# Kernel tuning notes

Hardware: AMD Instinct MI355X
Metric: run time of the kernel (lower is better)

The kernel has to match this reference:

```python
import jax, jax.numpy as jnp
import numpy as np

B, H, N, D = 64, 12, 196, 768  # ViT-B/16 @ 224: 196 patch tokens + 1 CLS


def setup_inputs() -> dict:
    key = jax.random.key(0)
    k1, k2, k3 = jax.random.split(key, 3)
    student_tokens = jax.random.normal(k1, (B, N, D), dtype=jnp.float32)
    teacher_tokens = jax.random.normal(k2, (B, N, D), dtype=jnp.float32)
    teacher_attn = jax.random.uniform(k3, (B, H, N + 1, N + 1), dtype=jnp.float32)
    return {
        "student_tokens": student_tokens,
        "teacher_tokens": teacher_tokens,
        "teacher_attn": teacher_attn,
    }


def reference(student_tokens, teacher_tokens, teacher_attn):
    s = student_tokens.astype(jnp.float32)
    t = teacher_tokens.astype(jnp.float32)
    # CLS->patch attention, averaged over heads: [B, N]
    w = teacher_attn[:, :, 0, 1:].mean(axis=1)
    w = w / (w.sum(axis=-1, keepdims=True) + 1e-8)
    s = w[..., None] * s
    t = w[..., None] * t
    # center over token dim
    s_c = s - s.mean(axis=1, keepdims=True)
    t_c = t - t.mean(axis=1, keepdims=True)
    tr_s = jnp.sum(s_c * s_c, axis=(1, 2))  # [B]
    tr_t = jnp.sum(t_c * t_c, axis=(1, 2))  # [B]
    # cross-covariance: [B, D, D]
    cross = jnp.einsum("bnd,bne->bde", s_c, t_c)
    # nuclear norm = sum of singular values
    nuclear = jnp.linalg.svd(cross, compute_uv=False).sum(axis=-1)  # [B]
    loss = jnp.maximum(tr_s + tr_t - 2.0 * nuclear, 0.0).mean()
    return loss
```

## Files before the change

### kernel.cpp

```cpp
#include <hip/hip_runtime.h>
#include <hip/hip_bf16.h>
#include <math.h>

#define NTOK 196
#define NDIM 768
#define NB 64
#define NH 12
#define NA 197
#define MAT (NTOK * NTOK)
#define ATTN_HW (NA * NA)
#define POLAR_ITERS 15

#define PADC 208
#define NTILE 13
#define POLAR_LDS_BYTES (2 * NTOK * PADC * 2)

#define GCH 64
#define GPLANE (208 * GCH)
#define GRAM_LDS_BYTES (2 * GPLANE * 2)

#define FCH 64
#define FA_ROWS 208
#define FB_ROWS 112
#define FAPLANE (FA_ROWS * FCH)
#define FBPLANE (FB_ROWS * FCH)
#define FMF_LDS_BYTES ((2 * FAPLANE + 2 * FBPLANE) * 2)

#define POW_LD 197
#define POW_F_WORDS (NTOK * POW_LD)
#define POW_LDS_BYTES ((POW_F_WORDS + 2 * NTOK + 256) * 4)

#define PTLD 208
#define TRI_WORDS 19306
#define CHOL2_PT_WORDS (16 * PTLD)
#define CHOL2_TRI_OFF CHOL2_PT_WORDS
#define CHOL2_ROWOFF_OFF (CHOL2_TRI_OFF + TRI_WORDS)
#define CHOL2_PV_OFF 22832
#define CHOL2_LDS_BYTES ((CHOL2_PV_OFF + 32) * 4)

typedef __attribute__((ext_vector_type(8))) short short8;
typedef __attribute__((ext_vector_type(4))) short short4_t;
typedef __attribute__((ext_vector_type(4))) float f32x4;

__device__ inline short8 s8zero() { short8 z = {0,0,0,0,0,0,0,0}; return z; }

__device__ inline short f2bf(float f) {
  union { float f; unsigned u; } v; v.f = f;
  unsigned u = v.u;
  u += 0x7fffu + ((u >> 16) & 1u);
  return (short)(u >> 16);
}
__device__ inline float bf2f(short s) {
  union { unsigned u; float f; } v;
  v.u = ((unsigned)(unsigned short)s) << 16;
  return v.f;
}

__global__ void k_w(const float* __restrict__ attn, float* __restrict__ wbuf) {
  int b = blockIdx.x;
  int tid = threadIdx.x;
  __shared__ float red[256];
  float w0 = 0.f;
  if (tid < NTOK) {
    size_t base = (size_t)b * NH * ATTN_HW + 1 + tid;
    #pragma unroll
    for (int h = 0; h < NH; ++h) w0 += attn[base + (size_t)h * ATTN_HW];
    w0 *= (1.f / NH);
  }
  red[tid] = (tid < NTOK) ? w0 : 0.f;
  __syncthreads();
  for (int s = 128; s > 0; s >>= 1) { if (tid < s) red[tid] += red[tid + s]; __syncthreads(); }
  float S = red[0];
  if (tid < NTOK) wbuf[b * NTOK + tid] = w0 / (S + 1e-8f);
}

__global__ __launch_bounds__(512, 1) void k_gram_mfma(
    const float* __restrict__ s, const float* __restrict__ t,
    const float* __restrict__ wbuf, float* __restrict__ Gbuf) {
  extern __shared__ short gsm[];
  short* bhp = gsm;
  short* blp = gsm + GPLANE;
  __shared__ float wsh[NTOK];
  int slot = blockIdx.x, b = slot >> 1, src = slot & 1;
  const float* X = (src ? t : s) + (size_t)b * NTOK * NDIM;
  int tid = threadIdx.x;
  int wave = tid >> 6, ln15 = tid & 15, quad = (tid >> 4) & 3;

  if (tid < NTOK) wsh[tid] = wbuf[b * NTOK + tid];
  for (int i = tid; i < 768; i += 512) {
    int p = i / 384, o = i - p * 384;
    ((int*)(gsm + p * GPLANE + 196 * GCH))[o] = 0;
  }
  __syncthreads();

  f32x4 zz = {0.f, 0.f, 0.f, 0.f};
  f32x4 acc[12];
  #pragma unroll
  for (int j = 0; j < 12; ++j) acc[j] = zz;

  for (int c = 0; c < NDIM / GCH; ++c) {
    int kc = c * GCH;
    for (int gi = tid; gi < NTOK * 8; gi += 512) {
      int r = gi >> 3, g = gi & 7;
      const float* sp = X + (size_t)r * NDIM + kc + g * 8;
      float4 f0 = *(const float4*)(sp);
      float4 f1 = *(const float4*)(sp + 4);
      float wv = wsh[r];
      float vs[8] = {f0.x, f0.y, f0.z, f0.w, f1.x, f1.y, f1.z, f1.w};
      short8 hv, lv;
      #pragma unroll
      for (int e = 0; e < 8; ++e) {
        float y = wv * vs[e];
        short hb = f2bf(y);
        hv[e] = hb;
        lv[e] = f2bf(y - bf2f(hb));
      }
      int pg = (g ^ (r & 7)) * 8;
      *(short8*)(bhp + r * GCH + pg) = hv;
      *(short8*)(blp + r * GCH + pg) = lv;
    }
    __syncthreads();
    #pragma unroll
    for (int j = 0; j < 12; ++j) {
      int T = wave + 8 * j;
      if (T < 91) {
        int ti = (int)((sqrtf(8.f * T + 1.f) - 1.f) * 0.5f);
        if ((ti + 1) * (ti + 2) / 2 <= T) ++ti;
        if (ti * (ti + 1) / 2 > T) --ti;
        int tj = T - ti * (ti + 1) / 2;
        int ra = ti * 16 + ln15, rb = tj * 16 + ln15;
        #pragma unroll
        for (int ks = 0; ks < 2; ++ks) {
          int gb0 = ks * 4 + quad;
          int ga = (gb0 ^ (ra & 7)) * 8, gb = (gb0 ^ (rb & 7)) * 8;
          short8 ah = *(const short8*)(bhp + ra * GCH + ga);
          short8 al = *(const short8*)(blp + ra * GCH + ga);
          short8 bhf = *(const short8*)(bhp + rb * GCH + gb);
          short8 blf = *(const short8*)(blp + rb * GCH + gb);
          acc[j] = __builtin_amdgcn_mfma_f32_16x16x32_bf16(ah, bhf, acc[j], 0, 0, 0);
          acc[j] = __builtin_amdgcn_mfma_f32_16x16x32_bf16(ah, blf, acc[j], 0, 0, 0);
          acc[j] = __builtin_amdgcn_mfma_f32_16x16x32_bf16(al, bhf, acc[j], 0, 0, 0);
        }
      }
    }
    __syncthreads();
  }

  float* G = Gbuf + (size_t)slot * MAT;
  #pragma unroll
  for (int j = 0; j < 12; ++j) {
    int T = wave + 8 * j;
    if (T < 91) {
      int ti = (int)((sqrtf(8.f * T + 1.f) - 1.f) * 0.5f);
      if ((ti + 1) * (ti + 2) / 2 <= T) ++ti;
      if (ti * (ti + 1) / 2 > T) --ti;
      int tj = T - ti * (ti + 1) / 2;
      int col = tj * 16 + ln15;
      #pragma unroll
      for (int r = 0; r < 4; ++r) {
        int row = ti * 16 + quad * 4 + r;
        if (row < NTOK && col < NTOK) {
          G[row * NTOK + col] = acc[j][r];
          if (ti != tj) G[col * NTOK + row] = acc[j][r];
        }
      }
    }
  }
}

__global__ void k_center(float* __restrict__ Gbuf, float* __restrict__ trPb) {
  int slot = blockIdx.x;
  float* A = Gbuf + (size_t)slot * MAT;
  __shared__ float r[NTOK];
  __shared__ float red[256];
  __shared__ float gsh, dsh;
  int tid = threadIdx.x;
  float acc = 0.f;
  if (tid < NTOK) {
    for (int m = 0; m < NTOK; ++m) acc += A[m * NTOK + tid];
    r[tid] = acc * (1.f / NTOK);
  }
  red[tid] = (tid < NTOK) ? acc * (1.f / NTOK) : 0.f;
  __syncthreads();
  for (int s = 128; s > 0; s >>= 1) { if (tid < s) red[tid] += red[tid + s]; __syncthreads(); }
  float g = red[0] * (1.f / NTOK);
  float tv = (tid < NTOK) ? (A[tid * NTOK + tid] - 2.f * r[tid] + g) : 0.f;
  __syncthreads();
  red[tid] = tv;
  __syncthreads();
  for (int s = 128; s > 0; s >>= 1) { if (tid < s) red[tid] += red[tid + s]; __syncthreads(); }
  if (tid == 0) {
    float tr = red[0];
    trPb[slot] = tr;
    gsh = g;
    dsh = 1e-4f * fmaxf(tr, 0.f) * (1.f / NTOK);
  }
  __syncthreads();
  float gg = gsh, dd = dsh;
  for (int idx = tid; idx < MAT; idx += 256) {
    int n = idx / NTOK, m = idx - n * NTOK;
    float v = A[idx] - r[n] - r[m] + gg;
    if (n == m) v += dd;
    A[idx] = v;
  }
}

__global__ __launch_bounds__(256, 1) void k_chol_panel(float* __restrict__ Gbuf,
                                                       int transposeOut) {
  extern __shared__ float smf[];
  float* Pt = smf;
  float* tri = smf + CHOL2_TRI_OFF;
  int* rowoff = (int*)(smf + CHOL2_ROWOFF_OFF);
  float* pvb = smf + CHOL2_PV_OFF;
  int slot = blockIdx.x;
  float* A = Gbuf + (size_t)slot * MAT;
  int tid = threadIdx.x;
  if (tid < NTOK) rowoff[tid] = tid * (tid + 1) / 2;
  __syncthreads();
  for (int idx = tid; idx < MAT; idx += 256) {
    int i = idx / NTOK, j = idx - i * NTOK;
    if (j <= i) tri[rowoff[i] + j] = A[idx];
  }
  __syncthreads();

  for (int k0 = 0; k0 < NTOK; k0 += 16) {
    int nb = (NTOK - k0 < 16) ? (NTOK - k0) : 16;
    int t = tid;
    int i = k0 + t;
    bool hasrow = (t < NTOK - k0);
    int ro = hasrow ? rowoff[i] : 0;

    float a[16];
    #pragma unroll
    for (int jj = 0; jj < 16; ++jj) a[jj] = 0.f;
    if (hasrow) {
      #pragma unroll
      for (int jj = 0; jj < 16; ++jj)
        if (jj < nb && k0 + jj <= i) a[jj] = tri[ro + k0 + jj];
    }

    #pragma unroll
    for (int jj = 0; jj < 16; ++jj) {
      bool cv = (jj < nb);
      if (cv && hasrow && t >= jj && t < nb) pvb[((jj & 1) << 4) + t] = a[jj];
      __syncthreads();
      if (cv && hasrow && t >= jj) {
        const float* pv = pvb + ((jj & 1) << 4);
        f32x4 p0 = *(const f32x4*)(pv);
        f32x4 p1 = *(const f32x4*)(pv + 4);
        f32x4 p2 = *(const f32x4*)(pv + 8);
        f32x4 p3 = *(const f32x4*)(pv + 12);
        float pvj = (jj < 4) ? p0[jj & 3] : (jj < 8) ? p1[jj & 3]
                   : (jj < 12) ? p2[jj & 3] : p3[jj & 3];
        float sq = sqrtf(fmaxf(pvj, 1e-20f));
        float pivinv = 1.f / sq;
        float v = a[jj] * pivinv;
        a[jj] = v;
        #pragma unroll
        for (int m = 0; m < 16; ++m) {
          if (m > jj) {
            float pvm = (m < 4) ? p0[m & 3] : (m < 8) ? p1[m & 3]
                       : (m < 12) ? p2[m & 3] : p3[m & 3];
            if (m < nb) a[m] -= v * (pvm * pivinv);
          }
        }
      }
    }

    if (hasrow) {
      #pragma unroll
      for (int jj = 0; jj < 16; ++jj)
        if (jj < nb && k0 + jj <= i) tri[ro + k0 + jj] = a[jj];
      if (t >= nb) {
        #pragma unroll
        for (int jj = 0; jj < 16; ++jj)
          if (jj < nb) Pt[jj * PTLD + i] = a[jj];
      }
    }
    __syncthreads();

    int k1 = k0 + nb;
    int nrem = NTOK - k1;
    if (nrem > 0) {
      int ntile = (nrem + 3) >> 2;
      int Ttot = ntile * (ntile + 1) / 2;
      for (int T = tid; T < Ttot; T += 256) {
        float disc = (2.f * ntile + 1.f) * (2.f * ntile + 1.f) - 8.f * (float)T;
        int tm = (int)((2.f * ntile + 1.f - sqrtf(fmaxf(disc, 0.f))) * 0.5f);
        if (tm > ntile - 1) tm = ntile - 1;
        if (tm < 0) tm = 0;
        #define FCOL(c) ((c) * ntile - (((c) * ((c) - 1)) >> 1))
        while (tm + 1 <= ntile - 1 && FCOL(tm + 1) <= T) ++tm;
        while (tm > 0 && FCOL(tm) > T) --tm;
        int ti = tm + (T - FCOL(tm));
        #undef FCOL
        int i0 = k1 + ti * 4, m0 = k1 + tm * 4;
        f32x4 acc0 = {0.f, 0.f, 0.f, 0.f};
        f32x4 acc1 = acc0, acc2 = acc0, acc3 = acc0;
        #pragma unroll
        for (int jj = 0; jj < 16; ++jj) {
          if (jj < nb) {
            f32x4 li = *(const f32x4*)(Pt + jj * PTLD + i0);
            f32x4 lm = *(const f32x4*)(Pt + jj * PTLD + m0);
            acc0 += lm * li[0];
            acc1 += lm * li[1];
            acc2 += lm * li[2];
            acc3 += lm * li[3];
          }
        }
        #define STORE_ROW(r, av)                                        \
          { int ii = i0 + (r);                                          \
            if (ii < NTOK) {                                            \
              int roi = rowoff[ii];                                     \
              if (m0 + 0 <= ii) tri[roi + m0 + 0] -= (av)[0];           \
              if (m0 + 1 <= ii) tri[roi + m0 + 1] -= (av)[1];           \
              if (m0 + 2 <= ii) tri[roi + m0 + 2] -= (av)[2];           \
              if (m0 + 3 <= ii) tri[roi + m0 + 3] -= (av)[3];           \
            } }
        STORE_ROW(0, acc0)
        STORE_ROW(1, acc1)
        STORE_ROW(2, acc2)
        STORE_ROW(3, acc3)
        #undef STORE_ROW
      }
    }
    __syncthreads();
  }

  if (transposeOut) {
    for (int idx = tid; idx < MAT; idx += 256) {
      int r2 = idx / NTOK, c2 = idx - r2 * NTOK;
      A[idx] = (r2 <= c2) ? tri[rowoff[c2] + r2] : 0.f;
    }
  } else {
    for (int idx = tid; idx < MAT; idx += 256) {
      int i = idx / NTOK, j = idx - i * NTOK;
      A[idx] = (j <= i) ? tri[rowoff[i] + j] : 0.f;
    }
  }
}

__global__ void k_chol_global(float* __restrict__ Gbuf) {
  int slot = blockIdx.x;
  float* A = Gbuf + (size_t)slot * MAT;
  __shared__ float col[NTOK];
  __shared__ float piv;
  int tid = threadIdx.x;
  for (int k = 0; k < NTOK; ++k) {
    if (tid == 0) { float p = sqrtf(fmaxf(A[k * NTOK + k], 1e-20f)); A[k * NTOK + k] = p; piv = p; }
    __syncthreads();
    float inv = 1.f / piv;
    for (int i = k + 1 + tid; i < NTOK; i += 256) {
      float v = A[i * NTOK + k] * inv;
      A[i * NTOK + k] = v;
      col[i] = v;
    }
    for (int j = k + 1 + tid; j < NTOK; j += 256) A[k * NTOK + j] = 0.f;
    __syncthreads();
    int nrem = NTOK - 1 - k;
    int total = nrem * (nrem + 1) / 2;
    for (int tt = tid; tt < total; tt += 256) {
      int a = (int)((sqrtf(8.f * tt + 1.f) - 1.f) * 0.5f);
      while ((a + 1) * (a + 2) / 2 <= tt) ++a;
      while (a * (a + 1) / 2 > tt) --a;
      int bb = tt - a * (a + 1) / 2;
      int i = k + 1 + a, j = k + 1 + bb;
      A[i * NTOK + j] -= col[i] * col[j];
    }
    __syncthreads();
  }
}

__global__ __launch_bounds__(512, 1) void k_F_mfma(const float* __restrict__ Gbuf,
                                                   float* __restrict__ Fbuf) {
  extern __shared__ short fsm[];
  short* Ah = fsm;
  short* Al = Ah + FAPLANE;
  short* Bh = Al + FAPLANE;
  short* Bl = Bh + FBPLANE;
  int half = blockIdx.x, b = blockIdx.y;
  const float* LTp = Gbuf + (size_t)(2 * b) * MAT;
  const float* LTq = Gbuf + (size_t)(2 * b + 1) * MAT;
  int co = half * 112;
  int tid = threadIdx.x;
  int wave = tid >> 6, ln15 = tid & 15, quad = (tid >> 4) & 3;

  f32x4 zz = {0.f, 0.f, 0.f, 0.f};
  f32x4 acc[12];
  #pragma unroll
  for (int j = 0; j < 12; ++j) acc[j] = zz;

  for (int c = 0; c < 4; ++c) {
    int kc = c * FCH;
    bool fullchunk = (kc + FCH <= NTOK);
    for (int gi = tid; gi < (FA_ROWS + FB_ROWS) * 8; gi += 512) {
      bool isA = gi < FA_ROWS * 8;
      int li = isA ? gi : gi - FA_ROWS * 8;
      int r = li >> 3, g = li & 7;
      int grow = isA ? r : co + r;
      short8 hv = s8zero(), lv = s8zero();
      if (grow < NTOK) {
        const float* src = (isA ? LTp : LTq) + (size_t)grow * NTOK + kc + g * 8;
        if (fullchunk) {
          float4 f0 = *(const float4*)(src);
          float4 f1 = *(const float4*)(src + 4);
          float vs[8] = {f0.x, f0.y, f0.z, f0.w, f1.x, f1.y, f1.z, f1.w};
          #pragma unroll
          for (int e = 0; e < 8; ++e) {
            short hb = f2bf(vs[e]);
            hv[e] = hb;
            lv[e] = f2bf(vs[e] - bf2f(hb));
          }
        } else {
          #pragma unroll
          for (int e = 0; e < 8; ++e) {
            int k = kc + g * 8 + e;
            if (k < NTOK) {
              float y = src[e];
              short hb = f2bf(y);
              hv[e] = hb;
              lv[e] = f2bf(y - bf2f(hb));
            }
          }
        }
      }
      int pg = (g ^ (r & 7)) * 8;
      if (isA) {
        *(short8*)(Ah + r * FCH + pg) = hv;
        *(short8*)(Al + r * FCH + pg) = lv;
      } else {
        *(short8*)(Bh + r * FCH + pg) = hv;
        *(short8*)(Bl + r * FCH + pg) = lv;
      }
    }
    __syncthreads();
    #pragma unroll
    for (int j = 0; j < 12; ++j) {
      int T = wave + 8 * j;
      if (T < 91) {
        int ti = T / 7, tj = T - ti * 7;
        if (co + tj * 16 < NTOK) {
          int ra = ti * 16 + ln15;
          int rb = tj * 16 + ln15;
          #pragma unroll
          for (int ks = 0; ks < 2; ++ks) {
            int gb0 = ks * 4 + quad;
            int ga = (gb0 ^ (ra & 7)) * 8, gb = (gb0 ^ (rb & 7)) * 8;
            short8 ah = *(const short8*)(Ah + ra * FCH + ga);
            short8 al = *(const short8*)(Al + ra * FCH + ga);
            short8 bh = *(const short8*)(Bh + rb * FCH + gb);
            short8 bl = *(const short8*)(Bl + rb * FCH + gb);
            acc[j] = __builtin_amdgcn_mfma_f32_16x16x32_bf16(ah, bh, acc[j], 0, 0, 0);
            acc[j] = __builtin_amdgcn_mfma_f32_16x16x32_bf16(ah, bl, acc[j], 0, 0, 0);
            acc[j] = __builtin_amdgcn_mfma_f32_16x16x32_bf16(al, bh, acc[j], 0, 0, 0);
          }
        }
      }
    }
    __syncthreads();
  }

  float* F = Fbuf + (size_t)b * MAT;
  #pragma unroll
  for (int j = 0; j < 12; ++j) {
    int T = wave + 8 * j;
    if (T < 91) {
      int ti = T / 7, tj = T - ti * 7;
      int col = co + tj * 16 + ln15;
      if (col < NTOK) {
        #pragma unroll
        for (int r = 0; r < 4; ++r) {
          int row = ti * 16 + quad * 4 + r;
          if (row < NTOK) F[row * NTOK + col] = acc[j][r];
        }
      }
    }
  }
}

__global__ void k_F(const float* __restrict__ Gbuf, float* __restrict__ Fbuf) {
  int b = blockIdx.y;
  const float* Lp = Gbuf + (size_t)(2 * b) * MAT;
  const float* Lq = Gbuf + (size_t)(2 * b + 1) * MAT;
  int ti = blockIdx.x / 7, tj = blockIdx.x % 7;
  int ri = ti * 32, cj = tj * 32;
  __shared__ float As[32][33], Bs[32][33];
  int tid = threadIdx.x, ty = tid >> 4, tx = tid & 15;
  float a00 = 0, a01 = 0, a10 = 0, a11 = 0;
  for (int k0 = 0; k0 < NTOK; k0 += 32) {
    for (int l = tid; l < 1024; l += 256) {
      int kk = l >> 5, ii = l & 31;
      int krow = k0 + kk;
      As[kk][ii] = (krow < NTOK && ri + ii < NTOK) ? Lp[(size_t)krow * NTOK + ri + ii] : 0.f;
      Bs[kk][ii] = (krow < NTOK && cj + ii < NTOK) ? Lq[(size_t)krow * NTOK + cj + ii] : 0.f;
    }
    __syncthreads();
    #pragma unroll
    for (int kk = 0; kk < 32; ++kk) {
      float p0 = As[kk][ty], p1 = As[kk][ty + 16];
      float q0 = Bs[kk][tx], q1 = Bs[kk][tx + 16];
      a00 += p0 * q0; a01 += p0 * q1; a10 += p1 * q0; a11 += p1 * q1;
    }
    __syncthreads();
  }
  float* F = Fbuf + (size_t)b * MAT;
  int i0 = ri + ty, i1 = ri + ty + 16, j0 = cj + tx, j1 = cj + tx + 16;
  if (i0 < NTOK && j0 < NTOK) F[i0 * NTOK + j0] = a00;
  if (i0 < NTOK && j1 < NTOK) F[i0 * NTOK + j1] = a01;
  if (i1 < NTOK && j0 < NTOK) F[i1 * NTOK + j0] = a10;
  if (i1 < NTOK && j1 < NTOK) F[i1 * NTOK + j1] = a11;
}

__global__ __launch_bounds__(256, 1) void k_pow_lds(const float* __restrict__ Fbuf,
                                                    float* __restrict__ nrmb) {
  extern __shared__ float psm[];
  float* Fsh = psm;
  float* v = psm + POW_F_WORDS;
  float* u = v + NTOK;
  float* red = u + NTOK;
  int b = blockIdx.x;
  const float* F = Fbuf + (size_t)b * MAT;
  int tid = threadIdx.x;
  for (int idx = tid; idx < MAT; idx += 256) {
    int i = idx / NTOK, j = idx - i * NTOK;
    Fsh[i * POW_LD + j] = F[idx];
  }
  if (tid < NTOK) v[tid] = 1.f;
  __syncthreads();
  float lastsum = 1.f;
  for (int it = 0; it < 6; ++it) {
    if (tid < NTOK) {
      float a = 0.f;
      for (int j = 0; j < NTOK; ++j) a += Fsh[tid * POW_LD + j] * v[j];
      u[tid] = a;
    }
    __syncthreads();
    float a2 = 0.f;
    if (tid < NTOK) { for (int i = 0; i < NTOK; ++i) a2 += Fsh[i * POW_LD + tid] * u[i]; }
    red[tid] = (tid < NTOK) ? a2 * a2 : 0.f;
    __syncthreads();
    for (int s2 = 128; s2 > 0; s2 >>= 1) { if (tid < s2) red[tid] += red[tid + s2]; __syncthreads(); }
    float sum = red[0];
    lastsum = sum;
    float invn = rsqrtf(sum + 1e-30f);
    __syncthreads();
    if (tid < NTOK) v[tid] = a2 * invn;
    __syncthreads();
  }
  if (tid == 0) {
    float sig = sqrtf(sqrtf(lastsum));
    nrmb[b] = 1.f / (1.1f * sig + 1e-30f);
  }
}

__global__ void k_pow(const float* __restrict__ Fbuf, float* __restrict__ nrmb) {
  int b = blockIdx.x;
  const float* F = Fbuf + (size_t)b * MAT;
  __shared__ float v[NTOK], u[NTOK];
  __shared__ float red[256];
  int tid = threadIdx.x;
  if (tid < NTOK) v[tid] = 1.f;
  __syncthreads();
  float lastsum = 1.f;
  for (int it = 0; it < 6; ++it) {
    float a = 0.f;
    if (tid < NTOK) { for (int j = 0; j < NTOK; ++j) a += F[tid * NTOK + j] * v[j]; }
    __syncthreads();
    if (tid < NTOK) u[tid] = a;
    __syncthreads();
    float a2 = 0.f;
    if (tid < NTOK) { for (int i = 0; i < NTOK; ++i) a2 += F[i * NTOK + tid] * u[i]; }
    red[tid] = (tid < NTOK) ? a2 * a2 : 0.f;
    __syncthreads();
    for (int s = 128; s > 0; s >>= 1) { if (tid < s) red[tid] += red[tid + s]; __syncthreads(); }
    float sum = red[0];
    lastsum = sum;
    float invn = rsqrtf(sum + 1e-30f);
    __syncthreads();
    if (tid < NTOK) v[tid] = a2 * invn;
    __syncthreads();
  }
  if (tid == 0) {
    float sig = sqrtf(sqrtf(lastsum));
    nrmb[b] = 1.f / (1.1f * sig + 1e-30f);
  }
}

__global__ void k_scale(const float* __restrict__ Fbuf, const float* __restrict__ nrmb,
                        float* __restrict__ X) {
  int b = blockIdx.y;
  int idx = blockIdx.x * 256 + threadIdx.x;
  if (idx < MAT) X[(size_t)b * MAT + idx] = Fbuf[(size_t)b * MAT + idx] * nrmb[b];
}

__global__ __launch_bounds__(512, 1) void k_polar_fused(
    const float* __restrict__ Fbuf, const float* __restrict__ nrmb,
    float* __restrict__ Xout) {
  extern __shared__ short sm[];
  short* bufA = sm;
  short* bufB = sm + NTOK * PADC;
  int b = blockIdx.x;
  const float* F = Fbuf + (size_t)b * MAT;
  float* XO = Xout + (size_t)b * MAT;
  int tid = threadIdx.x;
  int wave = tid >> 6, ln15 = tid & 15, quad = (tid >> 4) & 3;
  int rt0 = wave, rt1 = wave + 8;
  bool has2 = (rt1 < NTILE);

  for (int i = tid; i < (2 * NTOK * PADC) / 2; i += 512) ((int*)sm)[i] = 0;
  __syncthreads();
  float invc = nrmb[b];
  for (int idx = tid; idx < MAT; idx += 512) {
    int i = idx / NTOK, j = idx - i * NTOK;
    bufA[i * PADC + j] = f2bf(F[idx] * invc);
  }
  __syncthreads();

  int arow0 = rt0 * 16 + ln15;
  int arow1 = rt1 * 16 + ln15;
  bool av1 = has2 && (arow1 < NTOK);
  int m0a = rt0 * 16 + quad * 4;
  int m1a = rt1 * 16 + quad * 4;

  for (int it = 0; it < POLAR_ITERS; ++it) {
    {
      short8 a0[7], a1[7];
      #pragma unroll
      for (int ks = 0; ks < 7; ++ks) {
        int kk = ks * 32 + quad * 8;
        a0[ks] = (kk < PADC) ? *(const short8*)(bufA + arow0 * PADC + kk) : s8zero();
        a1[ks] = (av1 && kk < PADC) ? *(const short8*)(bufA + arow1 * PADC + kk) : s8zero();
      }
      for (int ct = 0; ct < NTILE; ++ct) {
        int brow = ct * 16 + ln15;
        bool bv = brow < NTOK;
        f32x4 acc0 = {0.f, 0.f, 0.f, 0.f};
        f32x4 acc1 = {0.f, 0.f, 0.f, 0.f};
        #pragma unroll
        for (int ks = 0; ks < 7; ++ks) {
          int kk = ks * 32 + quad * 8;
          short8 bfr = (bv && kk < PADC) ? *(const short8*)(bufA + brow * PADC + kk) : s8zero();
          acc0 = __builtin_amdgcn_mfma_f32_16x16x32_bf16(a0[ks], bfr, acc0, 0, 0, 0);
          if (has2)
            acc1 = __builtin_amdgcn_mfma_f32_16x16x32_bf16(a1[ks], bfr, acc1, 0, 0, 0);
        }
        if (bv) {
          short4_t w0;
          #pragma unroll
          for (int r = 0; r < 4; ++r) {
            float h = -0.5f * acc0[r] + ((m0a + r == brow) ? 1.5f : 0.f);
            w0[r] = f2bf(h);
          }
          *(short4_t*)(bufB + brow * PADC + m0a) = w0;
          if (has2) {
            short4_t w1;
            #pragma unroll
            for (int r = 0; r < 4; ++r) {
              float h = -0.5f * acc1[r] + ((m1a + r == brow) ? 1.5f : 0.f);
              w1[r] = f2bf(h);
            }
            *(short4_t*)(bufB + brow * PADC + m1a) = w1;
          }
        }
      }
    }
    __syncthreads();
    {
      short8 g0[7], g1[7];
      #pragma unroll
      for (int ks = 0; ks < 7; ++ks) {
        int kk = ks * 32 + quad * 8;
        short8 v0 = s8zero(), v1 = s8zero();
        if (kk < PADC) {
          #pragma unroll
          for (int j = 0; j < 8; ++j) {
            v0[j] = bufA[(kk + j) * PADC + arow0];
            if (has2) v1[j] = bufA[(kk + j) * PADC + arow1];
          }
        }
        g0[ks] = v0; g1[ks] = v1;
      }
      __syncthreads();
      for (int ct = 0; ct < NTILE; ++ct) {
        int n = ct * 16 + ln15;
        bool nv = n < NTOK;
        f32x4 acc0 = {0.f, 0.f, 0.f, 0.f};
        f32x4 acc1 = {0.f, 0.f, 0.f, 0.f};
        #pragma unroll
        for (int ks = 0; ks < 7; ++ks) {
          int kk = ks * 32 + quad * 8;
          short8 bfr = (nv && kk < PADC) ? *(const short8*)(bufB + n * PADC + kk) : s8zero();
          acc0 = __builtin_amdgcn_mfma_f32_16x16x32_bf16(g0[ks], bfr, acc0, 0, 0, 0);
          if (has2)
            acc1 = __builtin_amdgcn_mfma_f32_16x16x32_bf16(g1[ks], bfr, acc1, 0, 0, 0);
        }
        if (nv) {
          short4_t w0;
          #pragma unroll
          for (int r = 0; r < 4; ++r) w0[r] = f2bf(acc0[r]);
          *(short4_t*)(bufA + n * PADC + m0a) = w0;
          if (has2) {
            short4_t w1;
            #pragma unroll
            for (int r = 0; r < 4; ++r) w1[r] = f2bf(acc1[r]);
            *(short4_t*)(bufA + n * PADC + m1a) = w1;
          }
        }
      }
    }
    __syncthreads();
  }

  for (int idx = tid; idx < MAT; idx += 512) {
    int i = idx / NTOK, j = idx - i * NTOK;
    XO[idx] = bf2f(bufA[i * PADC + j]);
  }
}

__global__ void k_xtx(const float* __restrict__ Xb, float* __restrict__ Gp) {
  int b = blockIdx.y;
  const float* X = Xb + (size_t)b * MAT;
  int x = blockIdx.x, ti = 0;
  while (x >= ti + 1) { x -= ti + 1; ++ti; }
  int tj = x;
  int ri = ti * 32, cj = tj * 32;
  __shared__ float As[32][33], Bs[32][33];
  int tid = threadIdx.x, ty = tid >> 4, tx = tid & 15;
  float a00 = 0, a01 = 0, a10 = 0, a11 = 0;
  for (int k0 = 0; k0 < NTOK; k0 += 32) {
    for (int l = tid; l < 1024; l += 256) {
      int kk = l >> 5, ii = l & 31;
      int krow = k0 + kk;
      As[kk][ii] = (krow < NTOK && ri + ii < NTOK) ? X[(size_t)krow * NTOK + ri + ii] : 0.f;
      Bs[kk][ii] = (krow < NTOK && cj + ii < NTOK) ? X[(size_t)krow * NTOK + cj + ii] : 0.f;
    }
    __syncthreads();
    #pragma unroll
    for (int kk = 0; kk < 32; ++kk) {
      float p0 = As[kk][ty], p1 = As[kk][ty + 16];
      float q0 = Bs[kk][tx], q1 = Bs[kk][tx + 16];
      a00 += p0 * q0; a01 += p0 * q1; a10 += p1 * q0; a11 += p1 * q1;
    }
    __syncthreads();
  }
  float* G = Gp + (size_t)b * MAT;
  int i0 = ri + ty, i1 = ri + ty + 16, j0 = cj + tx, j1 = cj + tx + 16;
  if (i0 < NTOK && j0 < NTOK) { G[i0 * NTOK + j0] = a00; G[j0 * NTOK + i0] = a00; }
  if (i0 < NTOK && j1 < NTOK) { G[i0 * NTOK + j1] = a01; G[j1 * NTOK + i0] = a01; }
  if (i1 < NTOK && j0 < NTOK) { G[i1 * NTOK + j0] = a10; G[j0 * NTOK + i1] = a10; }
  if (i1 < NTOK && j1 < NTOK) { G[i1 * NTOK + j1] = a11; G[j1 * NTOK + i1] = a11; }
}

__global__ void k_nsup(const float* __restrict__ Xb, const float* __restrict__ Gp,
                       float* __restrict__ Xn) {
  int b = blockIdx.y;
  const float* X = Xb + (size_t)b * MAT;
  const float* G = Gp + (size_t)b * MAT;
  int ti = blockIdx.x / 7, tj = blockIdx.x % 7;
  int ri = ti * 32, cj = tj * 32;
  __shared__ float As[32][33], Bs[32][33];
  int tid = threadIdx.x, ty = tid >> 4, tx = tid & 15;
  float a00 = 0, a01 = 0, a10 = 0, a11 = 0;
  for (int k0 = 0; k0 < NTOK; k0 += 32) {
    for (int l = tid; l < 1024; l += 256) {
      int rr = l >> 5, cc = l & 31;
      As[rr][cc] = (ri + rr < NTOK && k0 + cc < NTOK) ? X[(size_t)(ri + rr) * NTOK + k0 + cc] : 0.f;
      Bs[rr][cc] = (k0 + rr < NTOK && cj + cc < NTOK) ? G[(size_t)(k0 + rr) * NTOK + cj + cc] : 0.f;
    }
    __syncthreads();
    #pragma unroll
    for (int kk = 0; kk < 32; ++kk) {
      float p0 = As[ty][kk], p1 = As[ty + 16][kk];
      float q0 = Bs[kk][tx], q1 = Bs[kk][tx + 16];
      a00 += p0 * q0; a01 += p0 * q1; a10 += p1 * q0; a11 += p1 * q1;
    }
    __syncthreads();
  }
  float* O = Xn + (size_t)b * MAT;
  int i0 = ri + ty, i1 = ri + ty + 16, j0 = cj + tx, j1 = cj + tx + 16;
  if (i0 < NTOK && j0 < NTOK) O[i0 * NTOK + j0] = 1.5f * X[i0 * NTOK + j0] - 0.5f * a00;
  if (i0 < NTOK && j1 < NTOK) O[i0 * NTOK + j1] = 1.5f * X[i0 * NTOK + j1] - 0.5f * a01;
  if (i1 < NTOK && j0 < NTOK) O[i1 * NTOK + j0] = 1.5f * X[i1 * NTOK + j0] - 0.5f * a10;
  if (i1 < NTOK && j1 < NTOK) O[i1 * NTOK + j1] = 1.5f * X[i1 * NTOK + j1] - 0.5f * a11;
}

__global__ void k_nuc(const float* __restrict__ U, const float* __restrict__ Fbuf,
                      float* __restrict__ nucb) {
  int b = blockIdx.x;
  int tid = threadIdx.x;
  const float* Ub = U + (size_t)b * MAT;
  const float* Fb = Fbuf + (size_t)b * MAT;
  float acc = 0.f;
  for (int idx = tid; idx < MAT; idx += 256) acc += Ub[idx] * Fb[idx];
  __shared__ float red[256];
  red[tid] = acc;
  __syncthreads();
  for (int s = 128; s > 0; s >>= 1) { if (tid < s) red[tid] += red[tid + s]; __syncthreads(); }
  if (tid == 0) nucb[b] = red[0];
}

__global__ void k_final(const float* __restrict__ trPb, const float* __restrict__ nucb,
                        float* __restrict__ out) {
  int tid = threadIdx.x;
  float v = fmaxf(trPb[2 * tid] + trPb[2 * tid + 1] - 2.f * nucb[tid], 0.f);
  #pragma unroll
  for (int off = 32; off; off >>= 1) v += __shfl_down(v, off);
  if (tid == 0) out[0] = v * (1.f / 64.f);
}

extern "C" void kernel_launch(void* const* d_in, const int* in_sizes, int n_in,
                              void* d_out, int out_size, void* d_ws, size_t ws_size,
                              hipStream_t stream) {
  (void)in_sizes; (void)n_in; (void)out_size; (void)ws_size;
  const float* s = (const float*)d_in[0];
  const float* t = (const float*)d_in[1];
  const float* attn = (const float*)d_in[2];
  float* out = (float*)d_out;

  float* W = (float*)d_ws;
  float* Gbuf = W;
  float* Fbuf = Gbuf + (size_t)128 * MAT;
  float* Xbuf = Fbuf + (size_t)64 * MAT;
  float* Xnew = Xbuf + (size_t)64 * MAT;
  float* Gpol = Xnew + (size_t)64 * MAT;
  float* wbuf = Gpol + (size_t)64 * MAT;
  float* trPb = wbuf + (size_t)NB * NTOK;
  float* nucb = trPb + 128;
  float* nrmb = nucb + 64;

  k_w<<<NB, 256, 0, stream>>>(attn, wbuf);
  k_gram_mfma<<<128, 512, GRAM_LDS_BYTES, stream>>>(s, t, wbuf, Gbuf);
  k_center<<<128, 256, 0, stream>>>(Gbuf, trPb);

  hipError_t chol_ok = hipFuncSetAttribute(
      reinterpret_cast<const void*>(k_chol_panel),
      hipFuncAttributeMaxDynamicSharedMemorySize, CHOL2_LDS_BYTES);
  hipError_t fmf_ok = hipFuncSetAttribute(
      reinterpret_cast<const void*>(k_F_mfma),
      hipFuncAttributeMaxDynamicSharedMemorySize, FMF_LDS_BYTES);
  bool mfmaF = (chol_ok == hipSuccess) && (fmf_ok == hipSuccess);

  if (chol_ok == hipSuccess) {
    k_chol_panel<<<128, 256, CHOL2_LDS_BYTES, stream>>>(Gbuf, mfmaF ? 1 : 0);
  } else {
    k_chol_global<<<128, 256, 0, stream>>>(Gbuf);
  }

  if (mfmaF) {
    k_F_mfma<<<dim3(2, 64), 512, FMF_LDS_BYTES, stream>>>(Gbuf, Fbuf);
  } else {
    k_F<<<dim3(49, 64), 256, 0, stream>>>(Gbuf, Fbuf);
  }

  hipError_t pow_ok = hipFuncSetAttribute(
      reinterpret_cast<const void*>(k_pow_lds),
      hipFuncAttributeMaxDynamicSharedMemorySize, POW_LDS_BYTES);
  if (pow_ok == hipSuccess) {
    k_pow_lds<<<64, 256, POW_LDS_BYTES, stream>>>(Fbuf, nrmb);
  } else {
    k_pow<<<64, 256, 0, stream>>>(Fbuf, nrmb);
  }

  hipError_t fused_ok = hipFuncSetAttribute(
      reinterpret_cast<const void*>(k_polar_fused),
      hipFuncAttributeMaxDynamicSharedMemorySize, POLAR_LDS_BYTES);

  const float* finalX;
  if (fused_ok == hipSuccess) {
    k_polar_fused<<<NB, 512, POLAR_LDS_BYTES, stream>>>(Fbuf, nrmb, Xbuf);
    k_xtx<<<dim3(28, 64), 256, 0, stream>>>(Xbuf, Gpol);
    k_nsup<<<dim3(49, 64), 256, 0, stream>>>(Xbuf, Gpol, Xnew);
    k_xtx<<<dim3(28, 64), 256, 0, stream>>>(Xnew, Gpol);
    k_nsup<<<dim3(49, 64), 256, 0, stream>>>(Xnew, Gpol, Xbuf);
    finalX = Xbuf;
  } else {
    k_scale<<<dim3(151, 64), 256, 0, stream>>>(Fbuf, nrmb, Xbuf);
    float* Xc = Xbuf;
    float* Xn = Xnew;
    for (int it = 0; it < POLAR_ITERS; ++it) {
      k_xtx<<<dim3(28, 64), 256, 0, stream>>>(Xc, Gpol);
      k_nsup<<<dim3(49, 64), 256, 0, stream>>>(Xc, Gpol, Xn);
      float* tmp = Xc; Xc = Xn; Xn = tmp;
    }
    finalX = Xc;
  }

  k_nuc<<<64, 256, 0, stream>>>(finalX, Fbuf, nucb);
  k_final<<<1, 64, 0, stream>>>(trPb, nucb, out);
}
```

Baseline: 944.4 us.

## Run polar polish iterations on MFMA with split-bf16 precision

Replaces the two fp32 SIMT Newton-Schulz polish iterations (k_xtx + k_nsup) with MFMA kernels that use hi/lo bf16 splitting. A Gram kernel forms X X^T using only the lower-triangle tiles, and the update kernel computes 1.5X - 0.5 H X from a transposed copy of X, which it also writes out for the next iteration. The goal is to cut the fp32 matmul cost of the polish step. The price is an extra transpose kernel, more workspace, and some accuracy loss from the 3-term bf16 split. The update kernel uses only 128 blocks.

```diff
diff --git a/kernel.cpp b/kernel.cpp
--- a/kernel.cpp
+++ b/kernel.cpp
@@ -25,6 +25,12 @@
 #define FAPLANE (FA_ROWS * FCH)
 #define FBPLANE (FB_ROWS * FCH)
 #define FMF_LDS_BYTES ((2 * FAPLANE + 2 * FBPLANE) * 2)
+
+#define HCH 64
+#define HPLANE (208 * HCH)
+#define H_LDS_BYTES (2 * HPLANE * 2)
+#define NS_SCR_BYTES (8 * 16 * 17 * 4)
+#define NS_LDS_BYTES (FMF_LDS_BYTES + NS_SCR_BYTES)
 
 #define POW_LD 197
 #define POW_F_WORDS (NTOK * POW_LD)
@@ -717,6 +723,257 @@
   }
 }
 
+__global__ void k_transpose(const float* __restrict__ Xb, float* __restrict__ Xt) {
+  int b = blockIdx.y;
+  int ti = blockIdx.x / 7, tj = blockIdx.x % 7;
+  const float* X = Xb + (size_t)b * MAT;
+  float* T = Xt + (size_t)b * MAT;
+  __shared__ float ts[32][33];
+  int tid = threadIdx.x;
+  int r = tid >> 5, c = tid & 31;
+  for (int rr = r; rr < 32; rr += 8) {
+    int gi = ti * 32 + rr, gj = tj * 32 + c;
+    ts[rr][c] = (gi < NTOK && gj < NTOK) ? X[gi * NTOK + gj] : 0.f;
+  }
+  __syncthreads();
+  for (int rr = r; rr < 32; rr += 8) {
+    int go = tj * 32 + rr, gc = ti * 32 + c;
+    if (go < NTOK && gc < NTOK) T[go * NTOK + gc] = ts[c][rr];
+  }
+}
+
+__global__ __launch_bounds__(512, 1) void k_h_mfma(const float* __restrict__ Xb,
+                                                   float* __restrict__ Hb) {
+  extern __shared__ short hsm[];
+  short* bhp = hsm;
+  short* blp = hsm + HPLANE;
+  int b = blockIdx.x;
+  const float* X = Xb + (size_t)b * MAT;
+  int tid = threadIdx.x;
+  int wave = tid >> 6, ln15 = tid & 15, quad = (tid >> 4) & 3;
+
+  for (int i = tid; i < 768; i += 512) {
+    int p = i / 384, o = i - p * 384;
+    ((int*)(hsm + p * HPLANE + 196 * HCH))[o] = 0;
+  }
+  __syncthreads();
+
+  f32x4 zz = {0.f, 0.f, 0.f, 0.f};
+  f32x4 acc[12];
+  #pragma unroll
+  for (int j = 0; j < 12; ++j) acc[j] = zz;
+
+  for (int c = 0; c < 4; ++c) {
+    int kc = c * HCH;
+    bool full = (kc + HCH <= NTOK);
+    for (int gi = tid; gi < NTOK * 8; gi += 512) {
+      int r = gi >> 3, g = gi & 7;
+      const float* sp = X + (size_t)r * NTOK + kc + g * 8;
+      short8 hv = s8zero(), lv = s8zero();
+      if (full) {
+        float4 f0 = *(const float4*)(sp);
+        float4 f1 = *(const float4*)(sp + 4);
+        float vs[8] = {f0.x, f0.y, f0.z, f0.w, f1.x, f1.y, f1.z, f1.w};
+        #pragma unroll
+        for (int e = 0; e < 8; ++e) {
+          short hb = f2bf(vs[e]);
+          hv[e] = hb;
+          lv[e] = f2bf(vs[e] - bf2f(hb));
+        }
+      } else {
+        #pragma unroll
+        for (int e = 0; e < 8; ++e) {
+          int k = kc + g * 8 + e;
+          if (k < NTOK) {
+            float y = sp[e];
+            short hb = f2bf(y);
+            hv[e] = hb;
+            lv[e] = f2bf(y - bf2f(hb));
+          }
+        }
+      }
+      int pg = (g ^ (r & 7)) * 8;
+      *(short8*)(bhp + r * HCH + pg) = hv;
+      *(short8*)(blp + r * HCH + pg) = lv;
+    }
+    __syncthreads();
+    #pragma unroll
+    for (int j = 0; j < 12; ++j) {
+      int T = wave + 8 * j;
+      if (T < 91) {
+        int ti = (int)((sqrtf(8.f * T + 1.f) - 1.f) * 0.5f);
+        if ((ti + 1) * (ti + 2) / 2 <= T) ++ti;
+        if (ti * (ti + 1) / 2 > T) --ti;
+        int tj = T - ti * (ti + 1) / 2;
+        int ra = ti * 16 + ln15, rb = tj * 16 + ln15;
+        #pragma unroll
+        for (int ks = 0; ks < 2; ++ks) {
+          int gb0 = ks * 4 + quad;
+          int ga = (gb0 ^ (ra & 7)) * 8, gb = (gb0 ^ (rb & 7)) * 8;
+          short8 ah = *(const short8*)(bhp + ra * HCH + ga);
+          short8 al = *(const short8*)(blp + ra * HCH + ga);
+          short8 bhf = *(const short8*)(bhp + rb * HCH + gb);
+          short8 blf = *(const short8*)(blp + rb * HCH + gb);
+          acc[j] = __builtin_amdgcn_mfma_f32_16x16x32_bf16(ah, bhf, acc[j], 0, 0, 0);
+          acc[j] = __builtin_amdgcn_mfma_f32_16x16x32_bf16(ah, blf, acc[j], 0, 0, 0);
+          acc[j] = __builtin_amdgcn_mfma_f32_16x16x32_bf16(al, bhf, acc[j], 0, 0, 0);
+        }
+      }
+    }
+    __syncthreads();
+  }
+
+  float* H = Hb + (size_t)b * MAT;
+  #pragma unroll
+  for (int j = 0; j < 12; ++j) {
+    int T = wave + 8 * j;
+    if (T < 91) {
+      int ti = (int)((sqrtf(8.f * T + 1.f) - 1.f) * 0.5f);
+      if ((ti + 1) * (ti + 2) / 2 <= T) ++ti;
+      if (ti * (ti + 1) / 2 > T) --ti;
+      int tj = T - ti * (ti + 1) / 2;
+      int col = tj * 16 + ln15;
+      #pragma unroll
+      for (int r = 0; r < 4; ++r) {
+        int row = ti * 16 + quad * 4 + r;
+        if (row < NTOK && col < NTOK) {
+          H[row * NTOK + col] = acc[j][r];
+          if (ti != tj) H[col * NTOK + row] = acc[j][r];
+        }
+      }
+    }
+  }
+}
+
+__global__ __launch_bounds__(512, 1) void k_nsup_mfma(
+    const float* __restrict__ Hb, const float* __restrict__ Wb,
+    const float* __restrict__ Xb, float* __restrict__ Xn,
+    float* __restrict__ Wn, int writeW) {
+  extern __shared__ short nsm[];
+  short* Ah = nsm;
+  short* Al = Ah + FAPLANE;
+  short* Bh = Al + FAPLANE;
+  short* Bl = Bh + FBPLANE;
+  float* scr = (float*)(nsm + 2 * FAPLANE + 2 * FBPLANE);
+  int half = blockIdx.x, b = blockIdx.y;
+  const float* H = Hb + (size_t)b * MAT;
+  const float* W = Wb + (size_t)b * MAT;
+  const float* X = Xb + (size_t)b * MAT;
+  int co = half * 112;
+  int tid = threadIdx.x;
+  int wave = tid >> 6, ln15 = tid & 15, quad = (tid >> 4) & 3;
+
+  f32x4 zz = {0.f, 0.f, 0.f, 0.f};
+  f32x4 acc[12];
+  #pragma unroll
+  for (int j = 0; j < 12; ++j) acc[j] = zz;
+
+  for (int c = 0; c < 4; ++c) {
+    int kc = c * FCH;
+    bool fullchunk = (kc + FCH <= NTOK);
+    for (int gi = tid; gi < (FA_ROWS + FB_ROWS) * 8; gi += 512) {
+      bool isA = gi < FA_ROWS * 8;
+      int li = isA ? gi : gi - FA_ROWS * 8;
+      int r = li >> 3, g = li & 7;
+      int grow = isA ? r : co + r;
+      short8 hv = s8zero(), lv = s8zero();
+      if (grow < NTOK) {
+        const float* src = (isA ? H : W) + (size_t)grow * NTOK + kc + g * 8;
+        if (fullchunk) {
+          float4 f0 = *(const float4*)(src);
+          float4 f1 = *(const float4*)(src + 4);
+          float vs[8] = {f0.x, f0.y, f0.z, f0.w, f1.x, f1.y, f1.z, f1.w};
+          #pragma unroll
+          for (int e = 0; e < 8; ++e) {
+            short hb = f2bf(vs[e]);
+            hv[e] = hb;
+            lv[e] = f2bf(vs[e] - bf2f(hb));
+          }
+        } else {
+          #pragma unroll
+          for (int e = 0; e < 8; ++e) {
+            int k = kc + g * 8 + e;
+            if (k < NTOK) {
+              float y = src[e];
+              short hb = f2bf(y);
+              hv[e] = hb;
+              lv[e] = f2bf(y - bf2f(hb));
+            }
+          }
+        }
+      }
+      int pg = (g ^ (r & 7)) * 8;
+      if (isA) {
+        *(short8*)(Ah + r * FCH + pg) = hv;
+        *(short8*)(Al + r * FCH + pg) = lv;
+      } else {
+        *(short8*)(Bh + r * FCH + pg) = hv;
+        *(short8*)(Bl + r * FCH + pg) = lv;
+      }
+    }
+    __syncthreads();
+    #pragma unroll
+    for (int j = 0; j < 12; ++j) {
+      int T = wave + 8 * j;
+      if (T < 91) {
+        int ti = T / 7, tj = T - ti * 7;
+        if (co + tj * 16 < NTOK) {
+          int ra = ti * 16 + ln15;
+          int rb = tj * 16 + ln15;
+          #pragma unroll
+          for (int ks = 0; ks < 2; ++ks) {
+            int gb0 = ks * 4 + quad;
+            int ga = (gb0 ^ (ra & 7)) * 8, gb = (gb0 ^ (rb & 7)) * 8;
+            short8 ah = *(const short8*)(Ah + ra * FCH + ga);
+            short8 al = *(const short8*)(Al + ra * FCH + ga);
+            short8 bh = *(const short8*)(Bh + rb * FCH + gb);
+            short8 bl = *(const short8*)(Bl + rb * FCH + gb);
+            acc[j] = __builtin_amdgcn_mfma_f32_16x16x32_bf16(ah, bh, acc[j], 0, 0, 0);
+            acc[j] = __builtin_amdgcn_mfma_f32_16x16x32_bf16(ah, bl, acc[j], 0, 0, 0);
+            acc[j] = __builtin_amdgcn_mfma_f32_16x16x32_bf16(al, bh, acc[j], 0, 0, 0);
+          }
+        }
+      }
+    }
+    __syncthreads();
+  }
+
+  float* XnB = Xn + (size_t)b * MAT;
+  float* WnB = writeW ? (Wn + (size_t)b * MAT) : (float*)0;
+  float* ws = scr + wave * 16 * 17;
+  #pragma unroll
+  for (int j = 0; j < 12; ++j) {
+    int T = wave + 8 * j;
+    if (T < 91) {
+      int ti = T / 7, tj = T - ti * 7;
+      int colbase = co + tj * 16;
+      if (colbase < NTOK) {
+        int col = colbase + ln15;
+        float vr[4];
+        #pragma unroll
+        for (int r = 0; r < 4; ++r) {
+          int row = ti * 16 + quad * 4 + r;
+          bool valid = (row < NTOK) && (col < NTOK);
+          float v = valid ? (1.5f * X[row * NTOK + col] - 0.5f * acc[j][r]) : 0.f;
+          vr[r] = v;
+          if (valid) XnB[row * NTOK + col] = v;
+        }
+        if (writeW) {
+          #pragma unroll
+          for (int r = 0; r < 4; ++r) ws[ln15 * 17 + quad * 4 + r] = vr[r];
+          #pragma unroll
+          for (int rr = 0; rr < 4; ++rr) {
+            int ro = colbase + quad * 4 + rr;
+            int cc = ti * 16 + ln15;
+            if (ro < NTOK && cc < NTOK)
+              WnB[ro * NTOK + cc] = ws[(quad * 4 + rr) * 17 + ln15];
+          }
+        }
+      }
+    }
+  }
+}
+
 __global__ void k_xtx(const float* __restrict__ Xb, float* __restrict__ Gp) {
   int b = blockIdx.y;
   const float* X = Xb + (size_t)b * MAT;
@@ -823,7 +1080,9 @@
   float* Xbuf = Fbuf + (size_t)64 * MAT;
   float* Xnew = Xbuf + (size_t)64 * MAT;
   float* Gpol = Xnew + (size_t)64 * MAT;
-  float* wbuf = Gpol + (size_t)64 * MAT;
+  float* Xt0  = Gpol + (size_t)64 * MAT;
+  float* Xt1  = Xt0 + (size_t)64 * MAT;
+  float* wbuf = Xt1 + (size_t)64 * MAT;
   float* trPb = wbuf + (size_t)NB * NTOK;
   float* nucb = trPb + 128;
   float* nrmb = nucb + 64;
@@ -864,14 +1123,29 @@
   hipError_t fused_ok = hipFuncSetAttribute(
       reinterpret_cast<const void*>(k_polar_fused),
       hipFuncAttributeMaxDynamicSharedMemorySize, POLAR_LDS_BYTES);
+  hipError_t h_ok = hipFuncSetAttribute(
+      reinterpret_cast<const void*>(k_h_mfma),
+      hipFuncAttributeMaxDynamicSharedMemorySize, H_LDS_BYTES);
+  hipError_t ns_ok = hipFuncSetAttribute(
+      reinterpret_cast<const void*>(k_nsup_mfma),
+      hipFuncAttributeMaxDynamicSharedMemorySize, NS_LDS_BYTES);
+  bool mfmaPolish = (h_ok == hipSuccess) && (ns_ok == hipSuccess);
 
   const float* finalX;
   if (fused_ok == hipSuccess) {
     k_polar_fused<<<NB, 512, POLAR_LDS_BYTES, stream>>>(Fbuf, nrmb, Xbuf);
-    k_xtx<<<dim3(28, 64), 256, 0, stream>>>(Xbuf, Gpol);
-    k_nsup<<<dim3(49, 64), 256, 0, stream>>>(Xbuf, Gpol, Xnew);
-    k_xtx<<<dim3(28, 64), 256, 0, stream>>>(Xnew, Gpol);
-    k_nsup<<<dim3(49, 64), 256, 0, stream>>>(Xnew, Gpol, Xbuf);
+    if (mfmaPolish) {
+      k_transpose<<<dim3(49, 64), 256, 0, stream>>>(Xbuf, Xt0);
+      k_h_mfma<<<64, 512, H_LDS_BYTES, stream>>>(Xbuf, Gpol);
+      k_nsup_mfma<<<dim3(2, 64), 512, NS_LDS_BYTES, stream>>>(Gpol, Xt0, Xbuf, Xnew, Xt1, 1);
+      k_h_mfma<<<64, 512, H_LDS_BYTES, stream>>>(Xnew, Gpol);
+      k_nsup_mfma<<<dim3(2, 64), 512, NS_LDS_BYTES, stream>>>(Gpol, Xt1, Xnew, Xbuf, (float*)0, 0);
+    } else {
+      k_xtx<<<dim3(28, 64), 256, 0, stream>>>(Xbuf, Gpol);
+      k_nsup<<<dim3(49, 64), 256, 0, stream>>>(Xbuf, Gpol, Xnew);
+      k_xtx<<<dim3(28, 64), 256, 0, stream>>>(Xnew, Gpol);
+      k_nsup<<<dim3(49, 64), 256, 0, stream>>>(Xnew, Gpol, Xbuf);
+    }
     finalX = Xbuf;
   } else {
     k_scale<<<dim3(151, 64), 256, 0, stream>>>(Fbuf, nrmb, Xbuf);
```

After: 888.8 us. -5.9%, faster.
